# Optimization experiments

Measured on AMD Instinct MI355X. Metric: run time of the kernel, lower is better.

The kernel has to match this reference:

```python
import jax, jax.numpy as jnp
import numpy as np


def setup_inputs() -> dict:
    key = jax.random.key(0)
    k1, k2 = jax.random.split(key)
    B, C, H, W = 4, 32, 512, 512
    inp = jax.random.normal(k1, (B, C, H, W), dtype=jnp.float32)
    # flow displacements of a few pixels, realistic for optical-flow warping
    flow = jax.random.normal(k2, (B, 2, H, W), dtype=jnp.float32) * 8.0
    return {"input": inp, "flow": flow}


def reference(input, flow):
    B, C, H, W = input.shape
    dt = input.dtype
    # meshgrid: grid[:,0]=x coords, grid[:,1]=y coords
    gx = jnp.arange(W, dtype=dt)[None, None, :]          # [1,1,W]
    gy = jnp.arange(H, dtype=dt)[None, :, None]          # [1,H,1]
    x = jnp.clip(gx + flow[:, 0], 0.0, W - 1).reshape(-1)  # [B*H*W]
    y = jnp.clip(gy + flow[:, 1], 0.0, H - 1).reshape(-1)

    x0f = jnp.floor(x)
    y0f = jnp.floor(y)
    x1f = x0f + 1.0
    y1f = y0f + 1.0
    x0 = x0f.astype(jnp.int32)
    y0 = y0f.astype(jnp.int32)
    x1 = jnp.clip(x1f, 0.0, W - 1).astype(jnp.int32)
    y1 = jnp.clip(y1f, 0.0, H - 1).astype(jnp.int32)

    base = jnp.repeat(jnp.arange(B, dtype=jnp.int32) * (H * W), H * W)
    base_y0 = base + y0 * W
    base_y1 = base + y1 * W

    img_flat = jnp.transpose(input, (0, 2, 3, 1)).reshape(-1, C)  # [B*H*W, C]
    Ia = img_flat[base_y0 + x0]
    Ib = img_flat[base_y1 + x0]
    Ic = img_flat[base_y0 + x1]
    Id = img_flat[base_y1 + x1]

    # bilinear weights (note: weights use unclamped x1f/y1f, matching original)
    wa = ((x1f - x) * (y1f - y))[:, None]
    wb = ((x1f - x) * (y - y0f))[:, None]
    wc = ((x - x0f) * (y1f - y))[:, None]
    wd = ((x - x0f) * (y - y0f))[:, None]

    out = wa * Ia + wb * Ib + wc * Ic + wd * Id            # [B*H*W, C]
    return jnp.transpose(out.reshape(B, H, W, C), (0, 3, 1, 2))
```

## Files before the change

### kernel.cpp

```cpp
#include <hip/hip_runtime.h>


constexpr int B = 4, C = 32, H = 512, W = 512;
constexpr int HW = H * W;
constexpr int TILE = 64;
constexpr int APRON = 31;
constexpr int RH = 128;
constexpr int RW = 128;
constexpr int BUF = RH * RW;

typedef __attribute__((address_space(1))) const unsigned int gas_u32;
typedef __attribute__((address_space(3))) unsigned int las_u32;

__global__ __launch_bounds__(1024, 1) void warp_tile_kernel(
    const float* __restrict__ input,
    const float* __restrict__ flow,
    float* __restrict__ out)
{
    __shared__ float s[2 * BUF];

    int bid0 = (int)blockIdx.x;
    int bid = (bid0 & 7) * 32 + (bid0 >> 3);

    int tx = bid & 7;
    int ty = (bid >> 3) & 7;
    int b  = bid >> 6;
    int tx0 = tx * TILE, ty0 = ty * TILE;

    int rx0 = tx0 - 32;
    int ry0 = ty0 - APRON;

    int tid  = (int)threadIdx.x;
    int lane = tid & 63;
    int wv   = tid >> 6;
    int cl   = tid & 63;
    int rl   = tid >> 6;

    int soff[4];
    int sr[4];
    {
        int lrow = lane >> 5;
        int lc   = (lane & 31) << 2;
        int gcol = min(max(rx0 + lc, 0), W - 4);
        #pragma unroll
        for (int i = 0; i < 4; ++i) {
            int r = 8 * wv + 2 * i;
            sr[i] = r;
            int grow = min(max(ry0 + r + lrow, 0), H - 1);
            soff[i] = grow * W + gcol;
        }
    }

    float wa[4], wb_[4], wc_[4], wd_[4];
    int a0[4], a1[4];
    int opix0 = (ty0 + rl) * W + tx0 + cl;

    #pragma unroll
    for (int p = 0; p < 4; ++p) {
        int h = ty0 + rl + 16 * p;
        int w = tx0 + cl;
        int pix = h * W + w;
        float fx = flow[(b * 2 + 0) * HW + pix];
        float fy = flow[(b * 2 + 1) * HW + pix];
        float x = fminf(fmaxf((float)w + fx, 0.0f), (float)(W - 1));
        float y = fminf(fmaxf((float)h + fy, 0.0f), (float)(H - 1));
        float x0f = floorf(x), y0f = floorf(y);
        int x0 = (int)x0f, y0 = (int)y0f;
        int y1 = min(y0 + 1, H - 1);
        float dx = x - x0f, dy = y - y0f;
        wa[p]  = (1.f - dx) * (1.f - dy);
        wb_[p] = (1.f - dx) * dy;
        wc_[p] = dx * (1.f - dy);
        wd_[p] = dx * dy;
        int ax0 = x0 - rx0, ay0 = y0 - ry0, ay1 = y1 - ry0;
        bool inreg = (ax0 >= 0) && (ax0 <= RW - 2) && (ay0 >= 0) && (ay1 <= RH - 1);
        a0[p] = inreg ? (ay0 * RW + ax0) : -1;
        a1[p] = ay1 * RW + ax0;
    }

    const float* iplane = input + (size_t)b * C * HW;
    float* oplane = out + (size_t)b * C * HW;

    auto stage = [&](int c, int buf) {
        const float* gc = iplane + (size_t)c * HW;
        #pragma unroll
        for (int i = 0; i < 4; ++i) {
            __builtin_amdgcn_global_load_lds(
                (gas_u32*)(gc + soff[i]),
                (las_u32*)(&s[buf * BUF + sr[i] * RW]),
                16, 0, 0);
        }
    };

    stage(0, 0);
    __syncthreads();

    for (int c = 0; c < C; ++c) {
        if (c + 1 < C) stage(c + 1, (c + 1) & 1);

        int base = (c & 1) * BUF;
        float v[4];
        #pragma unroll
        for (int p = 0; p < 4; ++p) {
            if (a0[p] >= 0) {
                int i0 = base + a0[p], i1 = base + a1[p];
                float v00 = s[i0], v01 = s[i0 + 1];
                float v10 = s[i1], v11 = s[i1 + 1];
                v[p] = wa[p] * v00 + wc_[p] * v01 + wb_[p] * v10 + wd_[p] * v11;
            } else {
                int h = ty0 + rl + 16 * p;
                int w = tx0 + cl;
                int pix = h * W + w;
                float fx = flow[(b * 2 + 0) * HW + pix];
                float fy = flow[(b * 2 + 1) * HW + pix];
                float x = fminf(fmaxf((float)w + fx, 0.0f), (float)(W - 1));
                float y = fminf(fmaxf((float)h + fy, 0.0f), (float)(H - 1));
                float x0f = floorf(x), y0f = floorf(y);
                int x0 = (int)x0f, y0 = (int)y0f;
                int x1 = min(x0 + 1, W - 1), y1 = min(y0 + 1, H - 1);
                float dx = x - x0f, dy = y - y0f;
                const float* pch = iplane + (size_t)c * HW;
                v[p] = (1.f - dx) * (1.f - dy) * pch[y0 * W + x0]
                     + (1.f - dx) * dy         * pch[y1 * W + x0]
                     + dx * (1.f - dy)         * pch[y0 * W + x1]
                     + dx * dy                 * pch[y1 * W + x1];
            }
        }

        asm volatile("s_waitcnt lgkmcnt(0)" ::: "memory");
        __builtin_amdgcn_sched_barrier(0);

        float* oc = oplane + (size_t)c * HW;
        #pragma unroll
        for (int p = 0; p < 4; ++p)
            oc[opix0 + 16 * p * W] = v[p];

        if (c + 1 < C) {
            asm volatile("s_waitcnt vmcnt(4)" ::: "memory");
            __builtin_amdgcn_sched_barrier(0);
            __builtin_amdgcn_s_barrier();
            __builtin_amdgcn_sched_barrier(0);
        }
    }
}

extern "C" void kernel_launch(void* const* d_in, const int* in_sizes, int n_in,
                              void* d_out, int out_size, void* d_ws, size_t ws_size,
                              hipStream_t stream) {
    const float* input = (const float*)d_in[0];
    const float* flow  = (const float*)d_in[1];
    float* out = (float*)d_out;

    int grid = B * (H / TILE) * (W / TILE);
    warp_tile_kernel<<<grid, 1024, 0, stream>>>(input, flow, out);
}
```

Baseline: 248.9 us.

## Shrink staged LDS region and precompute fallback gather addresses

Shrinks the per-channel LDS staging region from 128x128 to a 112x109 window with smaller aprons and loads it as flat 3x256-float chunks per wave instead of 4 row pairs, cutting the global-to-LDS traffic per channel. Out-of-region pixels now keep precomputed gather offsets and edge deltas, so the fallback path no longer reloads flow and recomputes coordinates every channel. The fallback global loads are also issued in a batch ahead of the LDS reads. The smaller apron means more pixels with large flow take the slower global path.

After: 249.3 us. Within noise of the previous version (+0.2%).

```diff
diff --git a/kernel.cpp b/kernel.cpp
--- a/kernel.cpp
+++ b/kernel.cpp
@@ -4,10 +4,10 @@
 constexpr int B = 4, C = 32, H = 512, W = 512;
 constexpr int HW = H * W;
 constexpr int TILE = 64;
-constexpr int APRON = 31;
-constexpr int RH = 128;
-constexpr int RW = 128;
-constexpr int BUF = RH * RW;
+constexpr int RW = 112;
+constexpr int RHF = 109;
+constexpr int BUFD = 12288;
+constexpr int XAP = 24, YAP = 22;
 
 typedef __attribute__((address_space(1))) const unsigned int gas_u32;
 typedef __attribute__((address_space(3))) unsigned int las_u32;
@@ -17,7 +17,7 @@
     const float* __restrict__ flow,
     float* __restrict__ out)
 {
-    __shared__ float s[2 * BUF];
+    __shared__ float s[2 * BUFD];
 
     int bid0 = (int)blockIdx.x;
     int bid = (bid0 & 7) * 32 + (bid0 >> 3);
@@ -27,8 +27,8 @@
     int b  = bid >> 6;
     int tx0 = tx * TILE, ty0 = ty * TILE;
 
-    int rx0 = tx0 - 32;
-    int ry0 = ty0 - APRON;
+    int rx0 = tx0 - XAP;
+    int ry0 = ty0 - YAP;
 
     int tid  = (int)threadIdx.x;
     int lane = tid & 63;
@@ -36,17 +36,18 @@
     int cl   = tid & 63;
     int rl   = tid >> 6;
 
-    int soff[4];
-    int sr[4];
+    int soff[3];
+    int sbase[3];
     {
-        int lrow = lane >> 5;
-        int lc   = (lane & 31) << 2;
-        int gcol = min(max(rx0 + lc, 0), W - 4);
         #pragma unroll
-        for (int i = 0; i < 4; ++i) {
-            int r = 8 * wv + 2 * i;
-            sr[i] = r;
-            int grow = min(max(ry0 + r + lrow, 0), H - 1);
+        for (int i = 0; i < 3; ++i) {
+            int base_ = (wv * 3 + i) * 256;
+            sbase[i] = base_;
+            int flat = base_ + 4 * lane;
+            int row = flat / RW;
+            int col = flat - row * RW;
+            int grow = min(max(ry0 + row, 0), H - 1);
+            int gcol = min(max(rx0 + col, 0), W - 4);
             soff[i] = grow * W + gcol;
         }
     }
@@ -66,65 +67,76 @@
         float y = fminf(fmaxf((float)h + fy, 0.0f), (float)(H - 1));
         float x0f = floorf(x), y0f = floorf(y);
         int x0 = (int)x0f, y0 = (int)y0f;
-        int y1 = min(y0 + 1, H - 1);
+        int x1 = min(x0 + 1, W - 1), y1 = min(y0 + 1, H - 1);
         float dx = x - x0f, dy = y - y0f;
         wa[p]  = (1.f - dx) * (1.f - dy);
         wb_[p] = (1.f - dx) * dy;
         wc_[p] = dx * (1.f - dy);
         wd_[p] = dx * dy;
         int ax0 = x0 - rx0, ay0 = y0 - ry0, ay1 = y1 - ry0;
-        bool inreg = (ax0 >= 0) && (ax0 <= RW - 2) && (ay0 >= 0) && (ay1 <= RH - 1);
-        a0[p] = inreg ? (ay0 * RW + ax0) : -1;
-        a1[p] = ay1 * RW + ax0;
+        bool inreg = (ax0 >= 0) && (ax0 <= RW - 2) && (ay0 >= 0) && (ay1 <= RHF - 1);
+        if (inreg) {
+            a0[p] = ay0 * RW + ax0;
+            a1[p] = ay1 * RW + ax0;
+        } else {
+            a0[p] = -1 - ((x1 - x0) + 2 * (y1 - y0));
+            a1[p] = y0 * W + x0;
+        }
     }
 
     const float* iplane = input + (size_t)b * C * HW;
     float* oplane = out + (size_t)b * C * HW;
 
-    auto stage = [&](int c, int buf) {
-        const float* gc = iplane + (size_t)c * HW;
-        #pragma unroll
-        for (int i = 0; i < 4; ++i) {
-            __builtin_amdgcn_global_load_lds(
-                (gas_u32*)(gc + soff[i]),
-                (las_u32*)(&s[buf * BUF + sr[i] * RW]),
-                16, 0, 0);
-        }
-    };
+    #define STAGE(cc, bb) do {                                          \
+        const float* gc_ = iplane + (size_t)(cc) * HW;                  \
+        _Pragma("unroll")                                               \
+        for (int i_ = 0; i_ < 3; ++i_) {                                \
+            __builtin_amdgcn_global_load_lds(                           \
+                (gas_u32*)(gc_ + soff[i_]),                             \
+                (las_u32*)(&s[(bb) * BUFD + sbase[i_]]),                \
+                16, 0, 0);                                              \
+        }                                                               \
+    } while (0)
 
-    stage(0, 0);
+    STAGE(0, 0);
     __syncthreads();
 
     for (int c = 0; c < C; ++c) {
-        if (c + 1 < C) stage(c + 1, (c + 1) & 1);
+        if (c + 1 < C) STAGE(c + 1, (c + 1) & 1);
+        __builtin_amdgcn_sched_barrier(0);
 
-        int base = (c & 1) * BUF;
+        int base = (c & 1) * BUFD;
+        const float* pch = iplane + (size_t)c * HW;
+
+        float f00[4], f01[4], f10[4], f11[4];
+        #pragma unroll
+        for (int p = 0; p < 4; ++p) {
+            if (a0[p] < 0) {
+                int e = -1 - a0[p];
+                int g00 = a1[p];
+                int g01 = g00 + (e & 1);
+                int g10 = g00 + ((e & 2) ? W : 0);
+                int g11 = g10 + (e & 1);
+                f00[p] = pch[g00];
+                f01[p] = pch[g01];
+                f10[p] = pch[g10];
+                f11[p] = pch[g11];
+            }
+        }
+
         float v[4];
         #pragma unroll
         for (int p = 0; p < 4; ++p) {
+            float v00, v01, v10, v11;
             if (a0[p] >= 0) {
                 int i0 = base + a0[p], i1 = base + a1[p];
-                float v00 = s[i0], v01 = s[i0 + 1];
-                float v10 = s[i1], v11 = s[i1 + 1];
-                v[p] = wa[p] * v00 + wc_[p] * v01 + wb_[p] * v10 + wd_[p] * v11;
+                v00 = s[i0]; v01 = s[i0 + 1];
+                v10 = s[i1]; v11 = s[i1 + 1];
             } else {
-                int h = ty0 + rl + 16 * p;
-                int w = tx0 + cl;
-                int pix = h * W + w;
-                float fx = flow[(b * 2 + 0) * HW + pix];
-                float fy = flow[(b * 2 + 1) * HW + pix];
-                float x = fminf(fmaxf((float)w + fx, 0.0f), (float)(W - 1));
-                float y = fminf(fmaxf((float)h + fy, 0.0f), (float)(H - 1));
-                float x0f = floorf(x), y0f = floorf(y);
-                int x0 = (int)x0f, y0 = (int)y0f;
-                int x1 = min(x0 + 1, W - 1), y1 = min(y0 + 1, H - 1);
-                float dx = x - x0f, dy = y - y0f;
-                const float* pch = iplane + (size_t)c * HW;
-                v[p] = (1.f - dx) * (1.f - dy) * pch[y0 * W + x0]
-                     + (1.f - dx) * dy         * pch[y1 * W + x0]
-                     + dx * (1.f - dy)         * pch[y0 * W + x1]
-                     + dx * dy                 * pch[y1 * W + x1];
+                v00 = f00[p]; v01 = f01[p];
+                v10 = f10[p]; v11 = f11[p];
             }
+            v[p] = wa[p] * v00 + wc_[p] * v01 + wb_[p] * v10 + wd_[p] * v11;
         }
 
         asm volatile("s_waitcnt lgkmcnt(0)" ::: "memory");
@@ -142,6 +154,7 @@
             __builtin_amdgcn_sched_barrier(0);
         }
     }
+    #undef STAGE
 }
 
 extern "C" void kernel_launch(void* const* d_in, const int* in_sizes, int n_in,
```
